# Kernel tuning notes

Hardware: AMD Instinct MI355X
Metric: run time of the kernel (lower is better)

## Reference

```python
import jax, jax.numpy as jnp
import numpy as np

B, C, I, E = 2048, 256, 9, 10


def _contraction(U_list, W_list, x, y):
    """Recursive symmetric contraction for one output irrep.
    U_list/W_list ordered [U1, U2, U3] (correlation 1..3).
    x: [b, c, i], y: [b, e]. Returns flattened [b, c * m].
    """
    U3, W3 = U_list[-1], W_list[-1]
    # main: '...ik,ekc,bci,be->bc...'
    out = jnp.einsum('...ik,ekc,bci,be->bc...', U3, W3, x, y)
    for corr in range(len(U_list) - 2, -1, -1):
        U, W = U_list[corr], W_list[corr]
        # weighting: '...k,ekc,be->bc...'
        c_tensor = jnp.einsum('...k,ekc,be->bc...', U, W, y) + out
        # contract: 'bc...i,bci->bc...'
        out = jnp.einsum('bc...i,bci->bc...', c_tensor, x)
    return out.reshape(out.shape[0], -1)


def setup_inputs() -> dict:
    key = jax.random.key(0)
    ks = jax.random.split(key, 14)
    inp = {
        'x': jax.random.normal(ks[0], (B, C, I), jnp.float32),
        'y': jax.random.uniform(ks[1], (B, E), jnp.float32),
        'U1_s': jax.random.normal(ks[2], (I, 1), jnp.float32),
        'U2_s': jax.random.normal(ks[3], (I, I, 3), jnp.float32),
        'U3_s': jax.random.normal(ks[4], (I, I, I, 23), jnp.float32),
        'U1_v': jax.random.normal(ks[5], (3, I, 1), jnp.float32),
        'U2_v': jax.random.normal(ks[6], (3, I, I, 4), jnp.float32),
        'U3_v': jax.random.normal(ks[7], (3, I, I, I, 30), jnp.float32),
        'W1_s': jax.random.normal(ks[8], (E, 1, C), jnp.float32),
        'W2_s': jax.random.normal(ks[9], (E, 3, C), jnp.float32) / 3.0,
        'W3_s': jax.random.normal(ks[10], (E, 23, C), jnp.float32) / 23.0,
        'W1_v': jax.random.normal(ks[11], (E, 1, C), jnp.float32),
        'W2_v': jax.random.normal(ks[12], (E, 4, C), jnp.float32) / 4.0,
        'W3_v': jax.random.normal(ks[13], (E, 30, C), jnp.float32) / 30.0,
    }
    return inp


def reference(x, y, U1_s, U2_s, U3_s, U1_v, U2_v, U3_v,
              W1_s, W2_s, W3_s, W1_v, W2_v, W3_v):
    out_s = _contraction([U1_s, U2_s, U3_s], [W1_s, W2_s, W3_s], x, y)  # [b, c]
    out_v = _contraction([U1_v, U2_v, U3_v], [W1_v, W2_v, W3_v], x, y)  # [b, c*3]
    return jnp.concatenate([out_s, out_v], axis=-1)  # [b, 4c]
```

## Files before the change

kernel.cpp:

```cpp
#include <hip/hip_runtime.h>
#include <hip/hip_bf16.h>


#define NB 2048
#define NC 256
#define NI 9
#define NE 10

#define N_TRI 165
#define N_PAIR 45
#define BT 8

#define T3N (N_TRI * NE * NC)
#define T2N (N_PAIR * NE * NC)
#define T1N (NI * NE * NC)
#define TBYTES ((size_t)(T3N + T2N + T1N) * 16)

#define MSPLIT 110

__global__ __launch_bounds__(256) void sc_prep(
    const float* __restrict__ U1_s, const float* __restrict__ U2_s,
    const float* __restrict__ U3_s, const float* __restrict__ U1_v,
    const float* __restrict__ U2_v, const float* __restrict__ U3_v,
    const float* __restrict__ W1_s, const float* __restrict__ W2_s,
    const float* __restrict__ W3_s, const float* __restrict__ W1_v,
    const float* __restrict__ W2_v, const float* __restrict__ W3_v,
    float* __restrict__ ws)
{
    const int m = blockIdx.x;
    const int tid = threadIdx.x;
    float4* __restrict__ T3 = (float4*)ws;
    float4* __restrict__ T2 = T3 + T3N;
    float4* __restrict__ T1 = T2 + T2N;

    __shared__ float sym[128];

    if (m < N_TRI) {
        if (tid < 113) {
            int ii = 0, jj = 0, kk = 0, cnt = 0;
            for (int i = 0; i < NI; i++)
                for (int j = i; j < NI; j++)
                    for (int k = j; k < NI; k++) {
                        if (cnt == m) { ii = i; jj = j; kk = k; }
                        cnt++;
                    }
            int P[6][3]; int np;
            if (ii == jj && jj == kk) {
                np = 1;
                P[0][0] = ii; P[0][1] = ii; P[0][2] = ii;
            } else if (ii == jj) {
                np = 3;
                P[0][0] = ii; P[0][1] = ii; P[0][2] = kk;
                P[1][0] = ii; P[1][1] = kk; P[1][2] = ii;
                P[2][0] = kk; P[2][1] = ii; P[2][2] = ii;
            } else if (jj == kk) {
                np = 3;
                P[0][0] = ii; P[0][1] = jj; P[0][2] = jj;
                P[1][0] = jj; P[1][1] = ii; P[1][2] = jj;
                P[2][0] = jj; P[2][1] = jj; P[2][2] = ii;
            } else {
                np = 6;
                P[0][0] = ii; P[0][1] = jj; P[0][2] = kk;
                P[1][0] = ii; P[1][1] = kk; P[1][2] = jj;
                P[2][0] = jj; P[2][1] = ii; P[2][2] = kk;
                P[3][0] = jj; P[3][1] = kk; P[3][2] = ii;
                P[4][0] = kk; P[4][1] = ii; P[4][2] = jj;
                P[5][0] = kk; P[5][1] = jj; P[5][2] = ii;
            }
            float s = 0.f;
            if (tid < 23) {
                for (int p = 0; p < np; p++)
                    s += U3_s[((P[p][0] * NI + P[p][1]) * NI + P[p][2]) * 23 + tid];
            } else {
                int a = (tid - 23) / 30, t = (tid - 23) % 30;
                for (int p = 0; p < np; p++)
                    s += U3_v[(((a * NI + P[p][0]) * NI + P[p][1]) * NI + P[p][2]) * 30 + t];
            }
            sym[tid] = s;
        }
        __syncthreads();
        const int c = tid;
        for (int e = 0; e < NE; e++) {
            float s = 0.f, v0 = 0.f, v1 = 0.f, v2 = 0.f;
            #pragma unroll
            for (int t = 0; t < 23; t++)
                s = fmaf(sym[t], W3_s[(e * 23 + t) * NC + c], s);
            #pragma unroll
            for (int t = 0; t < 30; t++) {
                float wv = W3_v[(e * 30 + t) * NC + c];
                v0 = fmaf(sym[23 + t], wv, v0);
                v1 = fmaf(sym[53 + t], wv, v1);
                v2 = fmaf(sym[83 + t], wv, v2);
            }
            T3[(m * NE + e) * NC + c] = make_float4(s, v0, v1, v2);
        }
    } else if (m < N_TRI + N_PAIR) {
        const int mm = m - N_TRI;
        if (tid < 15) {
            int ii = 0, jj = 0, cnt = 0;
            for (int i = 0; i < NI; i++)
                for (int j = i; j < NI; j++) {
                    if (cnt == mm) { ii = i; jj = j; }
                    cnt++;
                }
            float s;
            if (tid < 3) {
                s = U2_s[(ii * NI + jj) * 3 + tid];
                if (ii != jj) s += U2_s[(jj * NI + ii) * 3 + tid];
            } else {
                int a = (tid - 3) / 4, t = (tid - 3) % 4;
                s = U2_v[((a * NI + ii) * NI + jj) * 4 + t];
                if (ii != jj) s += U2_v[((a * NI + jj) * NI + ii) * 4 + t];
            }
            sym[tid] = s;
        }
        __syncthreads();
        const int c = tid;
        for (int e = 0; e < NE; e++) {
            float s = 0.f, v0 = 0.f, v1 = 0.f, v2 = 0.f;
            #pragma unroll
            for (int t = 0; t < 3; t++)
                s = fmaf(sym[t], W2_s[(e * 3 + t) * NC + c], s);
            #pragma unroll
            for (int t = 0; t < 4; t++) {
                float wv = W2_v[(e * 4 + t) * NC + c];
                v0 = fmaf(sym[3 + t],  wv, v0);
                v1 = fmaf(sym[7 + t],  wv, v1);
                v2 = fmaf(sym[11 + t], wv, v2);
            }
            T2[(mm * NE + e) * NC + c] = make_float4(s, v0, v1, v2);
        }
    } else {
        const int i = m - N_TRI - N_PAIR;
        const int c = tid;
        for (int e = 0; e < NE; e++) {
            float w1s = W1_s[e * NC + c], w1v = W1_v[e * NC + c];
            T1[(i * NE + e) * NC + c] = make_float4(
                U1_s[i] * w1s,
                U1_v[0 * NI + i] * w1v,
                U1_v[1 * NI + i] * w1v,
                U1_v[2 * NI + i] * w1v);
        }
    }
}

__device__ __forceinline__ void tri_advance(int& i, int& j, int& k) {
    k++;
    if (k == NI) { j++; if (j == NI) { i++; j = i; } k = j; }
}

#define ROW_FMA(BUF)                                              \
    {                                                             \
        _Pragma("unroll")                                         \
        for (int e = 0; e < NE; e++) {                            \
            const float4 t = BUF[e];                              \
            _Pragma("unroll")                                     \
            for (int n = 0; n < BT; n++) {                        \
                const float p = w[e][n] * phi[n];                 \
                acc[n][0] = fmaf(p, t.x, acc[n][0]);              \
                acc[n][1] = fmaf(p, t.y, acc[n][1]);              \
                acc[n][2] = fmaf(p, t.z, acc[n][2]);              \
                acc[n][3] = fmaf(p, t.w, acc[n][3]);              \
            }                                                     \
        }                                                         \
    }

template <int M0, int M1, int I0, int J0, int K0>
__device__ __forceinline__ void do_triples(
    const float4* __restrict__ T3, int c, const float* __restrict__ xb,
    const float (&w)[NE][BT], float (&acc)[BT][4])
{
    float4 bufA[NE], bufB[NE];
    #pragma unroll
    for (int e = 0; e < NE; e++) bufA[e] = T3[(M0 * NE + e) * NC + c];
    int i = I0, j = J0, k = K0;
    for (int m = M0; m + 1 < M1; m += 2) {
        #pragma unroll
        for (int e = 0; e < NE; e++) bufB[e] = T3[((m + 1) * NE + e) * NC + c];
        {
            float phi[BT];
            #pragma unroll
            for (int n = 0; n < BT; n++)
                phi[n] = xb[(i * BT + n) * 64] * xb[(j * BT + n) * 64]
                       * xb[(k * BT + n) * 64];
            ROW_FMA(bufA)
        }
        tri_advance(i, j, k);
        const int mp = (m + 2 < M1) ? m + 2 : M1 - 1;
        #pragma unroll
        for (int e = 0; e < NE; e++) bufA[e] = T3[(mp * NE + e) * NC + c];
        {
            float phi[BT];
            #pragma unroll
            for (int n = 0; n < BT; n++)
                phi[n] = xb[(i * BT + n) * 64] * xb[(j * BT + n) * 64]
                       * xb[(k * BT + n) * 64];
            ROW_FMA(bufB)
        }
        tri_advance(i, j, k);
    }
    if ((M1 - M0) & 1) {
        float phi[BT];
        #pragma unroll
        for (int n = 0; n < BT; n++)
            phi[n] = xb[(i * BT + n) * 64] * xb[(j * BT + n) * 64]
                   * xb[(k * BT + n) * 64];
        ROW_FMA(bufA)
    }
}

__global__ __launch_bounds__(128) void sc_main(
    const float* __restrict__ x, const float* __restrict__ y,
    const float* __restrict__ ws, float* __restrict__ out,
    float* __restrict__ pout, int full)
{
    const int tid = threadIdx.x;
    const int tx  = tid & 63;
    const int tyu = __builtin_amdgcn_readfirstlane(tid >> 6);
    const int bx  = blockIdx.x;
    const int part = blockIdx.y;
    const int xcd    = bx & 7;
    const int c_tile = xcd >> 1;
    const int b_tile = ((bx >> 3) << 1) | (xcd & 1);
    const int c  = (c_tile << 6) + tx;
    const int b0 = (b_tile << 4) + (tyu << 3);

    __shared__ float xs[2][NI][BT][64];
    #pragma unroll
    for (int n = 0; n < BT; n++) {
        const float* xp = x + ((size_t)(b0 + n) * NC + c) * NI;
        #pragma unroll
        for (int i = 0; i < NI; i++) xs[tyu][i][n][tx] = xp[i];
    }
    const float* xb = &xs[tyu][0][0][tx];

    float w[NE][BT];
    #pragma unroll
    for (int n = 0; n < BT; n++)
        #pragma unroll
        for (int e = 0; e < NE; e++) w[e][n] = y[(b0 + n) * NE + e];

    float acc[BT][4];
    #pragma unroll
    for (int n = 0; n < BT; n++)
        #pragma unroll
        for (int h = 0; h < 4; h++) acc[n][h] = 0.f;

    const float4* __restrict__ T3 = (const float4*)ws;
    const float4* __restrict__ T2 = T3 + T3N;
    const float4* __restrict__ T1 = T2 + T2N;

    const bool doA = full || part == 0;
    const bool doB = full || part == 1;

    if (doA)
        do_triples<0, MSPLIT, 0, 0, 0>(T3, c, xb, w, acc);

    if (doB) {
        do_triples<MSPLIT, N_TRI, 3, 3, 4>(T3, c, xb, w, acc);

        {
            float4 bufA[NE], bufB[NE];
            #pragma unroll
            for (int e = 0; e < NE; e++) bufA[e] = T2[e * NC + c];
            int i = 0, j = 0;
            for (int m = 0; m + 1 < N_PAIR; m += 2) {
                #pragma unroll
                for (int e = 0; e < NE; e++) bufB[e] = T2[((m + 1) * NE + e) * NC + c];
                {
                    float phi[BT];
                    #pragma unroll
                    for (int n = 0; n < BT; n++)
                        phi[n] = xb[(i * BT + n) * 64] * xb[(j * BT + n) * 64];
                    ROW_FMA(bufA)
                }
                j++; if (j == NI) { i++; j = i; }
                const int mp = (m + 2 < N_PAIR) ? m + 2 : N_PAIR - 1;
                #pragma unroll
                for (int e = 0; e < NE; e++) bufA[e] = T2[(mp * NE + e) * NC + c];
                {
                    float phi[BT];
                    #pragma unroll
                    for (int n = 0; n < BT; n++)
                        phi[n] = xb[(i * BT + n) * 64] * xb[(j * BT + n) * 64];
                    ROW_FMA(bufB)
                }
                j++; if (j == NI) { i++; j = i; }
            }
            {
                float phi[BT];
                #pragma unroll
                for (int n = 0; n < BT; n++)
                    phi[n] = xb[(i * BT + n) * 64] * xb[(j * BT + n) * 64];
                ROW_FMA(bufA)
            }
        }

        for (int i = 0; i < NI; i++) {
            float4 tc[NE];
            #pragma unroll
            for (int e = 0; e < NE; e++) tc[e] = T1[(i * NE + e) * NC + c];
            float phi[BT];
            #pragma unroll
            for (int n = 0; n < BT; n++) phi[n] = xb[(i * BT + n) * 64];
            ROW_FMA(tc)
        }
    }

    float* __restrict__ dst = (!full && part == 0) ? pout : out;
    #pragma unroll
    for (int n = 0; n < BT; n++) {
        float* ob = dst + (size_t)(b0 + n) * (4 * NC);
        ob[c] = acc[n][0];
        ob[NC + 3 * c + 0] = acc[n][1];
        ob[NC + 3 * c + 1] = acc[n][2];
        ob[NC + 3 * c + 2] = acc[n][3];
    }
}

__global__ __launch_bounds__(256) void sc_combine(
    float4* __restrict__ out, const float4* __restrict__ p, int n4)
{
    int i = blockIdx.x * 256 + threadIdx.x;
    if (i < n4) {
        float4 a = out[i], b = p[i];
        out[i] = make_float4(a.x + b.x, a.y + b.y, a.z + b.z, a.w + b.w);
    }
}

extern "C" void kernel_launch(void* const* d_in, const int* in_sizes, int n_in,
                              void* d_out, int out_size, void* d_ws, size_t ws_size,
                              hipStream_t stream) {
    const float* x    = (const float*)d_in[0];
    const float* y    = (const float*)d_in[1];
    const float* U1_s = (const float*)d_in[2];
    const float* U2_s = (const float*)d_in[3];
    const float* U3_s = (const float*)d_in[4];
    const float* U1_v = (const float*)d_in[5];
    const float* U2_v = (const float*)d_in[6];
    const float* U3_v = (const float*)d_in[7];
    const float* W1_s = (const float*)d_in[8];
    const float* W2_s = (const float*)d_in[9];
    const float* W3_s = (const float*)d_in[10];
    const float* W1_v = (const float*)d_in[11];
    const float* W2_v = (const float*)d_in[12];
    const float* W3_v = (const float*)d_in[13];
    float* out = (float*)d_out;
    float* ws  = (float*)d_ws;

    const size_t out_bytes = (size_t)out_size * sizeof(float);
    const bool split = ws_size >= TBYTES + out_bytes;
    float* pout = (float*)((char*)d_ws + TBYTES);

    sc_prep<<<N_TRI + N_PAIR + NI, 256, 0, stream>>>(
        U1_s, U2_s, U3_s, U1_v, U2_v, U3_v,
        W1_s, W2_s, W3_s, W1_v, W2_v, W3_v, ws);

    if (split) {
        sc_main<<<dim3(512, 2), 128, 0, stream>>>(x, y, ws, out, pout, 0);
        const int n4 = out_size / 4;
        sc_combine<<<(n4 + 255) / 256, 256, 0, stream>>>(
            (float4*)out, (const float4*)pout, n4);
    } else {
        sc_main<<<dim3(512, 1), 128, 0, stream>>>(x, y, ws, out, out, 1);
    }
}
```

Baseline: 328.6 us.

## Split triple range across two waves per block with in-LDS reduction

Instead of splitting the triple-product work across a second grid dimension and then summing partial outputs in a separate combine kernel, each block now covers one 8-batch tile. Its two waves take the two halves of the work and reduce through shared memory. This removes the partial-output round trip to global memory and the extra combine launch, and both waves share a single cooperatively loaded x tile. The cost is a block-level barrier, and a block now finishes only when its slower wave does, since the halves may be imbalanced.

```diff
diff --git a/kernel.cpp b/kernel.cpp
--- a/kernel.cpp
+++ b/kernel.cpp
@@ -14,7 +14,6 @@
 #define T3N (N_TRI * NE * NC)
 #define T2N (N_PAIR * NE * NC)
 #define T1N (NI * NE * NC)
-#define TBYTES ((size_t)(T3N + T2N + T1N) * 16)
 
 #define MSPLIT 110
 
@@ -211,28 +210,32 @@
 
 __global__ __launch_bounds__(128) void sc_main(
     const float* __restrict__ x, const float* __restrict__ y,
-    const float* __restrict__ ws, float* __restrict__ out,
-    float* __restrict__ pout, int full)
+    const float* __restrict__ ws, float* __restrict__ out)
 {
     const int tid = threadIdx.x;
     const int tx  = tid & 63;
-    const int tyu = __builtin_amdgcn_readfirstlane(tid >> 6);
-    const int bx  = blockIdx.x;
-    const int part = blockIdx.y;
-    const int xcd    = bx & 7;
+    const int wv  = __builtin_amdgcn_readfirstlane(tid >> 6);
+    const int bid = blockIdx.x;
+    const int xcd    = bid & 7;
     const int c_tile = xcd >> 1;
-    const int b_tile = ((bx >> 3) << 1) | (xcd & 1);
-    const int c  = (c_tile << 6) + tx;
-    const int b0 = (b_tile << 4) + (tyu << 3);
-
-    __shared__ float xs[2][NI][BT][64];
+    const int b_tile = ((bid >> 3) << 1) | (xcd & 1);
+    const int c0 = c_tile << 6;
+    const int c  = c0 + tx;
+    const int b0 = b_tile << 3;
+
+    __shared__ float xs[NI][BT][64];
+    __shared__ float red[BT][4][64];
+
     #pragma unroll
-    for (int n = 0; n < BT; n++) {
-        const float* xp = x + ((size_t)(b0 + n) * NC + c) * NI;
-        #pragma unroll
-        for (int i = 0; i < NI; i++) xs[tyu][i][n][tx] = xp[i];
-    }
-    const float* xb = &xs[tyu][0][0][tx];
+    for (int p = 0; p < 4; p++) {
+        const int pair = tid + p * 128;
+        const int n = pair >> 6, cc = pair & 63;
+        const float* xp = x + ((size_t)(b0 + n) * NC + c0 + cc) * NI;
+        #pragma unroll
+        for (int i = 0; i < NI; i++) xs[i][n][cc] = xp[i];
+    }
+    __syncthreads();
+    const float* xb = &xs[0][0][tx];
 
     float w[NE][BT];
     #pragma unroll
@@ -250,13 +253,9 @@
     const float4* __restrict__ T2 = T3 + T3N;
     const float4* __restrict__ T1 = T2 + T2N;
 
-    const bool doA = full || part == 0;
-    const bool doB = full || part == 1;
-
-    if (doA)
+    if (wv == 0) {
         do_triples<0, MSPLIT, 0, 0, 0>(T3, c, xb, w, acc);
-
-    if (doB) {
+    } else {
         do_triples<MSPLIT, N_TRI, 3, 3, 4>(T3, c, xb, w, acc);
 
         {
@@ -307,24 +306,22 @@
         }
     }
 
-    float* __restrict__ dst = (!full && part == 0) ? pout : out;
-    #pragma unroll
-    for (int n = 0; n < BT; n++) {
-        float* ob = dst + (size_t)(b0 + n) * (4 * NC);
-        ob[c] = acc[n][0];
-        ob[NC + 3 * c + 0] = acc[n][1];
-        ob[NC + 3 * c + 1] = acc[n][2];
-        ob[NC + 3 * c + 2] = acc[n][3];
-    }
-}
-
-__global__ __launch_bounds__(256) void sc_combine(
-    float4* __restrict__ out, const float4* __restrict__ p, int n4)
-{
-    int i = blockIdx.x * 256 + threadIdx.x;
-    if (i < n4) {
-        float4 a = out[i], b = p[i];
-        out[i] = make_float4(a.x + b.x, a.y + b.y, a.z + b.z, a.w + b.w);
+    if (wv == 0) {
+        #pragma unroll
+        for (int n = 0; n < BT; n++)
+            #pragma unroll
+            for (int h = 0; h < 4; h++) red[n][h][tx] = acc[n][h];
+    }
+    __syncthreads();
+    if (wv == 1) {
+        #pragma unroll
+        for (int n = 0; n < BT; n++) {
+            float* ob = out + (size_t)(b0 + n) * (4 * NC);
+            ob[c]              = acc[n][0] + red[n][0][tx];
+            ob[NC + 3 * c + 0] = acc[n][1] + red[n][1][tx];
+            ob[NC + 3 * c + 1] = acc[n][2] + red[n][2][tx];
+            ob[NC + 3 * c + 2] = acc[n][3] + red[n][3][tx];
+        }
     }
 }
 
@@ -348,20 +345,8 @@
     float* out = (float*)d_out;
     float* ws  = (float*)d_ws;
 
-    const size_t out_bytes = (size_t)out_size * sizeof(float);
-    const bool split = ws_size >= TBYTES + out_bytes;
-    float* pout = (float*)((char*)d_ws + TBYTES);
-
     sc_prep<<<N_TRI + N_PAIR + NI, 256, 0, stream>>>(
         U1_s, U2_s, U3_s, U1_v, U2_v, U3_v,
         W1_s, W2_s, W3_s, W1_v, W2_v, W3_v, ws);
-
-    if (split) {
-        sc_main<<<dim3(512, 2), 128, 0, stream>>>(x, y, ws, out, pout, 0);
-        const int n4 = out_size / 4;
-        sc_combine<<<(n4 + 255) / 256, 256, 0, stream>>>(
-            (float4*)out, (const float4*)pout, n4);
-    } else {
-        sc_main<<<dim3(512, 1), 128, 0, stream>>>(x, y, ws, out, out, 1);
-    }
-}
+    sc_main<<<1024, 128, 0, stream>>>(x, y, ws, out);
+}
```

After: 340.4 us. 1.04x slower.
